# Performance work log

Measured on AMD Instinct MI355X. Metric: run time of the kernel, lower is better.

Reference implementation:

```python
import jax, jax.numpy as jnp
import numpy as np

B, H, W, D, K = 16, 64, 64, 128, 4096


def setup_inputs() -> dict:
    key = jax.random.key(0)
    k1, k2 = jax.random.split(key)
    z = jax.random.normal(k1, (B, H, W, D), dtype=jnp.float32)
    emb = jax.random.normal(k2, (K, D), dtype=jnp.float32)
    return {"z": z, "emb": emb}


def reference(z, emb):
    # z: [B,H,W,D] pre-quantized features (channels-last, as in the torch code
    # after permute(0,2,3,1)); emb: [K,D] codebook.
    d = z.shape[-1]
    zf = z.reshape(-1, d)  # [N,D]
    # squared euclidean distances: ||z||^2 + ||e||^2 - 2 z.e
    dists = (jnp.sum(zf * zf, axis=1, keepdims=True)
             + jnp.sum(emb * emb, axis=1)
             - 2.0 * zf @ emb.T)  # [N,K]
    idx = jnp.argmin(dists, axis=1)  # [N]
    # one-hot @ emb in the original == direct gather (same math)
    z_q = jnp.take(emb, idx, axis=0).reshape(z.shape)  # [B,H,W,D]
    codebook_loss = jnp.mean((jax.lax.stop_gradient(z_q) - z) ** 2)
    commitment_loss = jnp.mean((z_q - jax.lax.stop_gradient(z)) ** 2)
    loss = codebook_loss + 0.25 * commitment_loss
    # straight-through estimator
    z_q_st = z + jax.lax.stop_gradient(z_q - z)
    z_q_out = jnp.transpose(z_q_st, (0, 3, 1, 2))  # [B,D,H,W]
    return z_q_out, loss
```

## Files before the change

### kernel.cpp

```cpp
#include <hip/hip_runtime.h>

#define NB 16
#define NH 64
#define NW 64
#define ND 128
#define NK 4096
#define NROWS (NB * NH * NW)
#define OUT_ELEMS (NB * ND * NH * NW)
#define MARGIN_F 0.10f

typedef _Float16 f16x8 __attribute__((ext_vector_type(8)));
typedef float f32x4 __attribute__((ext_vector_type(4)));

__device__ __forceinline__ unsigned short f2h(float x) {
    _Float16 h = (_Float16)x;
    return __builtin_bit_cast(unsigned short, h);
}
__device__ __forceinline__ unsigned long long pack_si(float s, int idx) {
    unsigned int u = __float_as_uint(s);
    unsigned int key = ((int)u < 0) ? ~u : (u | 0x80000000u);
    return ((unsigned long long)key << 32) | (unsigned int)idx;
}

__global__ void emb_prep_kernel(const float* __restrict__ emb,
                                float* __restrict__ enorm,
                                unsigned short* __restrict__ e_h) {
    int wave = (blockIdx.x * blockDim.x + threadIdx.x) >> 6;
    int lane = threadIdx.x & 63;
    if (wave >= NK) return;
    const float* e = emb + (size_t)wave * ND;
    float a = e[lane];
    float b = e[lane + 64];
    const int m = (wave & 7) << 3;
    e_h[(size_t)wave * ND + (lane ^ m)] = f2h(a);
    e_h[(size_t)wave * ND + ((lane + 64) ^ m)] = f2h(b);
    float s = a * a + b * b;
#pragma unroll
    for (int off = 32; off > 0; off >>= 1) s += __shfl_down(s, off, 64);
    if (lane == 0) enorm[wave] = s;
}

#define ZST 136

__global__ void
__attribute__((amdgpu_flat_work_group_size(256, 256)))
mfma_argmin_kernel(const float* __restrict__ z,
                   const unsigned short* __restrict__ e_h,
                   const float* __restrict__ enorm,
                   int* __restrict__ idx_out,
                   int* __restrict__ rcount,
                   int* __restrict__ rlist,
                   unsigned long long* __restrict__ rpart) {
    __shared__ alignas(16) unsigned short ubuf[2 * 64 * ND];
    __shared__ float redb1[2 * 64];
    __shared__ float redb2[2 * 64];
    __shared__ int   redi1[2 * 64];

    const int bid = blockIdx.x;
    const int rowbase = bid * 64;
    const int t = threadIdx.x;
    const int lane = t & 63;
    const int wid = __builtin_amdgcn_readfirstlane(t >> 6);

    const float4* zg = (const float4*)(z + (size_t)rowbase * ND);
#pragma unroll
    for (int q = 0; q < 8; q++) {
        int i = t + 256 * q;
        float4 v = zg[i];
        int r = i >> 5;
        int c4 = (i & 31) << 2;
        ushort4 hv = make_ushort4(f2h(v.x), f2h(v.y), f2h(v.z), f2h(v.w));
        *(ushort4*)&ubuf[r * ZST + c4] = hv;
    }
    __syncthreads();

    const int quad = lane >> 4;
    const int c = lane & 15;
    const int rh = wid >> 1;
    const int ch = wid & 1;

    f16x8 ar[2][4];
#pragma unroll
    for (int mi = 0; mi < 2; mi++)
#pragma unroll
        for (int kk = 0; kk < 4; kk++)
            ar[mi][kk] = *(const f16x8*)&ubuf[(rh * 32 + mi * 16 + c) * ZST + quad * 8 + kk * 32];
    __syncthreads();

#pragma unroll
    for (int j = 0; j < 4; j++) {
        int seg = (wid << 2) + j;
        __builtin_amdgcn_global_load_lds(
            (const unsigned int*)(e_h + seg * 512 + lane * 8),
            (unsigned int*)&ubuf[seg * 512], 16, 0, 0);
    }
    float en0 = enorm[ch * 32 + c];
    float en1 = enorm[ch * 32 + 16 + c];
    __syncthreads();

    const int bswz = (c & 7) << 3;
    const int bbase0 = (ch * 32 + c) * ND;

    float b1[2][4], b2[2][4];
    int i1[2][4];
#pragma unroll
    for (int mi = 0; mi < 2; mi++)
#pragma unroll
        for (int r = 0; r < 4; r++) { b1[mi][r] = -3.4e38f; b2[mi][r] = -3.4e38f; i1[mi][r] = 0; }

    for (int ts = 0; ts < NK / 64; ts++) {
        const int cur = ts & 1;
        const int curoff = cur << 13;

        float nen0 = 0.f, nen1 = 0.f;
        if (ts < NK / 64 - 1) {
            nen0 = enorm[(ts + 1) * 64 + ch * 32 + c];
            nen1 = enorm[(ts + 1) * 64 + ch * 32 + 16 + c];
            const unsigned short* gt = e_h + (size_t)(ts + 1) * (64 * ND);
#pragma unroll
            for (int j = 0; j < 4; j++) {
                int seg = (wid << 2) + j;
                __builtin_amdgcn_global_load_lds(
                    (const unsigned int*)(gt + seg * 512 + lane * 8),
                    (unsigned int*)&ubuf[(curoff ^ 8192) + seg * 512], 16, 0, 0);
            }
        }

        const float h0 = -0.5f * en0;
        const float h1 = -0.5f * en1;
        f32x4 acc[2][2];
#pragma unroll
        for (int mi = 0; mi < 2; mi++) {
            acc[mi][0] = (f32x4){h0, h0, h0, h0};
            acc[mi][1] = (f32x4){h1, h1, h1, h1};
        }

#pragma unroll
        for (int kk = 0; kk < 4; kk++) {
            const int doff = (quad * 8 + kk * 32) ^ bswz;
            f16x8 bv0 = *(const f16x8*)&ubuf[curoff + bbase0 + doff];
            f16x8 bv1 = *(const f16x8*)&ubuf[curoff + bbase0 + 16 * ND + doff];
            acc[0][0] = __builtin_amdgcn_mfma_f32_16x16x32_f16(ar[0][kk], bv0, acc[0][0], 0, 0, 0);
            acc[0][1] = __builtin_amdgcn_mfma_f32_16x16x32_f16(ar[0][kk], bv1, acc[0][1], 0, 0, 0);
            acc[1][0] = __builtin_amdgcn_mfma_f32_16x16x32_f16(ar[1][kk], bv0, acc[1][0], 0, 0, 0);
            acc[1][1] = __builtin_amdgcn_mfma_f32_16x16x32_f16(ar[1][kk], bv1, acc[1][1], 0, 0, 0);
        }

#pragma unroll
        for (int ni = 0; ni < 2; ni++) {
            const int n = ts * 64 + ch * 32 + ni * 16 + c;
#pragma unroll
            for (int mi = 0; mi < 2; mi++)
#pragma unroll
                for (int r = 0; r < 4; r++) {
                    float q = acc[mi][ni][r];
                    b2[mi][r] = fmaxf(b2[mi][r], fminf(b1[mi][r], q));
                    i1[mi][r] = (q > b1[mi][r]) ? n : i1[mi][r];
                    b1[mi][r] = fmaxf(b1[mi][r], q);
                }
        }

        __syncthreads();
        en0 = nen0;
        en1 = nen1;
    }

#pragma unroll
    for (int off = 1; off < 16; off <<= 1) {
#pragma unroll
        for (int mi = 0; mi < 2; mi++)
#pragma unroll
            for (int r = 0; r < 4; r++) {
                float ob1 = __shfl_xor(b1[mi][r], off, 64);
                float ob2 = __shfl_xor(b2[mi][r], off, 64);
                int oi1 = __shfl_xor(i1[mi][r], off, 64);
                float hi = fmaxf(b1[mi][r], ob1);
                float lo = fminf(b1[mi][r], ob1);
                b2[mi][r] = fmaxf(fmaxf(b2[mi][r], ob2), lo);
                i1[mi][r] = (ob1 > b1[mi][r]) ? oi1 : i1[mi][r];
                b1[mi][r] = hi;
            }
    }

    if (c == 0) {
#pragma unroll
        for (int mi = 0; mi < 2; mi++)
#pragma unroll
            for (int r = 0; r < 4; r++) {
                int rowl = rh * 32 + mi * 16 + quad * 4 + r;
                redb1[ch * 64 + rowl] = b1[mi][r];
                redb2[ch * 64 + rowl] = b2[mi][r];
                redi1[ch * 64 + rowl] = i1[mi][r];
            }
    }
    __syncthreads();

    if (t < 64) {
        float B1 = redb1[t], B2 = redb2[t];
        int I1 = redi1[t];
        float ob1 = redb1[64 + t];
        float ob2 = redb2[64 + t];
        int oi1 = redi1[64 + t];
        float hi = fmaxf(B1, ob1);
        float lo = fminf(B1, ob1);
        B2 = fmaxf(fmaxf(B2, ob2), lo);
        I1 = (ob1 > B1) ? oi1 : I1;
        B1 = hi;
        idx_out[rowbase + t] = I1;
        if (2.0f * (B1 - B2) < MARGIN_F) {
            rpart[rowbase + t] = ~0ull;
            int p = atomicAdd(rcount, 1);
            rlist[p] = rowbase + t;
        }
    }
}

#define RR 8
#define SC 512
#define CH 64

__global__ void __launch_bounds__(256, 2)
rescue_kernel(const float* __restrict__ z,
              const float* __restrict__ emb,
              const float* __restrict__ enorm,
              const int* __restrict__ rcount,
              const int* __restrict__ rlist,
              unsigned long long* __restrict__ rpart) {
    __shared__ float2 ze[RR * 64];
    __shared__ float2 es[64 * 65];
    __shared__ int ids[RR];

    const int t = threadIdx.x;
    const int cnt = *rcount;
    if (cnt == 0) return;
    const int ngrp = (cnt + RR - 1) / RR;
    const int nwork = ngrp * 8;

    const int r = t >> 6;
    const int cl = t & 63;

    for (int g = blockIdx.x; g < nwork; g += gridDim.x) {
        const int gi = g >> 3;
        const int slice = g & 7;

        if (t < RR) {
            int j = gi * RR + t;
            ids[t] = rlist[j < cnt ? j : cnt - 1];
        }
        __syncthreads();
        const int rowA = ids[r];
        const int rowB = ids[r + 4];
#pragma unroll
        for (int q2 = 0; q2 < 2; q2++) {
            int i = t + 256 * q2;
            int rr = i >> 6;
            int d2 = i & 63;
            ze[rr * 64 + d2] = ((const float2*)(z + (size_t)ids[rr] * ND))[d2];
        }

        unsigned long long bestA = ~0ull, bestB = ~0ull;
        const int kbase = slice * SC;

        for (int ch2 = 0; ch2 < SC / CH; ch2++) {
            __syncthreads();
#pragma unroll
            for (int q = 0; q < 16; q++) {
                int i = t + 256 * q;
                int code = i >> 6;
                int d2 = i & 63;
                float2 v = ((const float2*)(emb + (size_t)(kbase + ch2 * CH + code) * ND))[d2];
                es[d2 * 65 + code] = v;
            }
            __syncthreads();

            int k = kbase + ch2 * CH + cl;
            float a0 = 0.f, a1 = 0.f, a2 = 0.f, a3 = 0.f;
            float c0 = 0.f, c1 = 0.f, c2 = 0.f, c3 = 0.f;
#pragma unroll
            for (int d2 = 0; d2 < 64; d2 += 2) {
                float2 ev0 = es[d2 * 65 + cl];
                float2 ev1 = es[(d2 + 1) * 65 + cl];
                float2 zA0 = ze[r * 64 + d2];
                float2 zA1 = ze[r * 64 + d2 + 1];
                float2 zB0 = ze[(r + 4) * 64 + d2];
                float2 zB1 = ze[(r + 4) * 64 + d2 + 1];
                a0 = fmaf(zA0.x, ev0.x, a0);
                a1 = fmaf(zA0.y, ev0.y, a1);
                a2 = fmaf(zA1.x, ev1.x, a2);
                a3 = fmaf(zA1.y, ev1.y, a3);
                c0 = fmaf(zB0.x, ev0.x, c0);
                c1 = fmaf(zB0.y, ev0.y, c1);
                c2 = fmaf(zB1.x, ev1.x, c2);
                c3 = fmaf(zB1.y, ev1.y, c3);
            }
            float sA = fmaf(-2.0f, (a0 + a1) + (a2 + a3), enorm[k]);
            float sB = fmaf(-2.0f, (c0 + c1) + (c2 + c3), enorm[k]);
            unsigned long long pA = pack_si(sA, k);
            unsigned long long pB = pack_si(sB, k);
            bestA = (pA < bestA) ? pA : bestA;
            bestB = (pB < bestB) ? pB : bestB;
        }

#pragma unroll
        for (int off = 32; off > 0; off >>= 1) {
            unsigned long long oA = __shfl_down(bestA, off, 64);
            unsigned long long oB = __shfl_down(bestB, off, 64);
            bestA = (oA < bestA) ? oA : bestA;
            bestB = (oB < bestB) ? oB : bestB;
        }
        if (cl == 0) {
            atomicMin(&rpart[rowA], bestA);
            atomicMin(&rpart[rowB], bestB);
        }
        __syncthreads();
    }
}

__global__ void rescue_fin_kernel(const int* __restrict__ rcount,
                                  const int* __restrict__ rlist,
                                  const unsigned long long* __restrict__ rpart,
                                  int* __restrict__ idx_out) {
    const int cnt = *rcount;
    for (int i = blockIdx.x * blockDim.x + threadIdx.x; i < cnt;
         i += gridDim.x * blockDim.x) {
        int row = rlist[i];
        idx_out[row] = (int)(rpart[row] & 0xffffffffull);
    }
}

__global__ void out_kernel(const float* __restrict__ z,
                           const float* __restrict__ emb,
                           const int* __restrict__ idx,
                           float* __restrict__ out,
                           float* __restrict__ losspart) {
    __shared__ float zq[64 * 129];
    __shared__ int ids[64];
    __shared__ float redl[4];

    const int bid = blockIdx.x;
    const int b = bid >> 6;
    const int h = bid & 63;
    const int rowbase = bid * 64;
    const int t = threadIdx.x;

    if (t < 64) ids[t] = idx[rowbase + t];
    __syncthreads();

    const int d = t & 127;
    const int w0 = t >> 7;
    float lsum = 0.f;
#pragma unroll
    for (int wq = 0; wq < 32; wq++) {
        int w = w0 + 2 * wq;
        float e = emb[(size_t)ids[w] * ND + d];
        float zv = z[((size_t)(rowbase + w)) * ND + d];
        float df = e - zv;
        lsum = fmaf(df, df, lsum);
        zq[w * 129 + d] = e;
    }
#pragma unroll
    for (int off = 32; off > 0; off >>= 1) lsum += __shfl_down(lsum, off, 64);
    if ((t & 63) == 0) redl[t >> 6] = lsum;
    __syncthreads();
    if (t == 0) losspart[bid] = redl[0] + redl[1] + redl[2] + redl[3];

    const int w = t & 63;
    const int dq = t >> 6;
#pragma unroll
    for (int dd0 = 0; dd0 < 32; dd0++) {
        int dd = dq + 4 * dd0;
        out[(((size_t)b * ND + dd) * NH + h) * NW + w] = zq[w * 129 + dd];
    }
}

__global__ void loss_kernel(const float* __restrict__ losspart,
                            float* __restrict__ out) {
    __shared__ float redl[4];
    const int t = threadIdx.x;
    float s = 0.f;
#pragma unroll
    for (int i = 0; i < 4; i++) s += losspart[t + 256 * i];
#pragma unroll
    for (int off = 32; off > 0; off >>= 1) s += __shfl_down(s, off, 64);
    if ((t & 63) == 0) redl[t >> 6] = s;
    __syncthreads();
    if (t == 0) {
        float total = redl[0] + redl[1] + redl[2] + redl[3];
        out[OUT_ELEMS] = 1.25f * total / (float)OUT_ELEMS;
    }
}

extern "C" void kernel_launch(void* const* d_in, const int* in_sizes, int n_in,
                              void* d_out, int out_size, void* d_ws, size_t ws_size,
                              hipStream_t stream) {
    const float* z = (const float*)d_in[0];
    const float* emb = (const float*)d_in[1];
    float* out = (float*)d_out;

    char* ws = (char*)d_ws;
    int* ws_idx = (int*)ws;
    float* ws_enorm = (float*)(ws + (256 << 10));
    float* ws_losspart = (float*)(ws + (272 << 10));
    int* ws_rcount = (int*)(ws + (276 << 10));
    int* ws_rlist = (int*)(ws + (277 << 10));
    unsigned short* ws_eh = (unsigned short*)(ws + (533 << 10));
    unsigned long long* ws_rpart = (unsigned long long*)(ws + (1557 << 10));

    hipMemsetAsync(ws_rcount, 0, sizeof(int), stream);
    emb_prep_kernel<<<NK / 4, 256, 0, stream>>>(emb, ws_enorm, ws_eh);
    mfma_argmin_kernel<<<NROWS / 64, 256, 0, stream>>>(z, ws_eh, ws_enorm,
                                                       ws_idx, ws_rcount,
                                                       ws_rlist, ws_rpart);
    rescue_kernel<<<2048, 256, 0, stream>>>(z, emb, ws_enorm, ws_rcount,
                                            ws_rlist, ws_rpart);
    rescue_fin_kernel<<<64, 256, 0, stream>>>(ws_rcount, ws_rlist, ws_rpart,
                                              ws_idx);
    out_kernel<<<NB * NH, 256, 0, stream>>>(z, emb, ws_idx, out, ws_losspart);
    loss_kernel<<<1, 256, 0, stream>>>(ws_losspart, out);
}
```

Measured before the change: 325.9 us.

## Pre-transpose codebook and double-buffer rescue tiles via direct global-to-LDS loads

Adds a kernel that transposes the fp32 codebook into a d-major float2 layout once. The rescue kernel then streams 64-code chunks from it straight into LDS with global_load_lds, double-buffered so the next chunk loads while the current one is computed. This replaces the per-chunk register-staged transposed store and removes one barrier per chunk. In exchange it costs an extra launch, about 2 MB of transpose traffic, and doubled LDS use. It also drops the launch-bounds occupancy hint.

```diff
diff --git a/kernel.cpp b/kernel.cpp
--- a/kernel.cpp
+++ b/kernel.cpp
@@ -38,6 +38,28 @@
 #pragma unroll
     for (int off = 32; off > 0; off >>= 1) s += __shfl_down(s, off, 64);
     if (lane == 0) enorm[wave] = s;
+}
+
+__global__ void transp_kernel(const float* __restrict__ emb,
+                              float2* __restrict__ emb_t) {
+    __shared__ float2 tile[64 * 65];
+    const int cb = blockIdx.x * 64;
+    const int t = threadIdx.x;
+#pragma unroll
+    for (int q = 0; q < 16; q++) {
+        int i = t + 256 * q;
+        int code = i >> 6;
+        int d2 = i & 63;
+        tile[code * 65 + d2] = ((const float2*)(emb + (size_t)(cb + code) * ND))[d2];
+    }
+    __syncthreads();
+#pragma unroll
+    for (int q = 0; q < 16; q++) {
+        int i = t + 256 * q;
+        int d2 = i >> 6;
+        int code = i & 63;
+        emb_t[(size_t)d2 * NK + cb + code] = tile[code * 65 + d2];
+    }
 }
 
 #define ZST 136
@@ -219,15 +241,15 @@
 #define SC 512
 #define CH 64
 
-__global__ void __launch_bounds__(256, 2)
+__global__ void
 rescue_kernel(const float* __restrict__ z,
-              const float* __restrict__ emb,
+              const float2* __restrict__ emb_t,
               const float* __restrict__ enorm,
               const int* __restrict__ rcount,
               const int* __restrict__ rlist,
               unsigned long long* __restrict__ rpart) {
+    __shared__ alignas(16) float2 es[2][64 * 64];
     __shared__ float2 ze[RR * 64];
-    __shared__ float2 es[64 * 65];
     __shared__ int ids[RR];
 
     const int t = threadIdx.x;
@@ -258,28 +280,40 @@
             ze[rr * 64 + d2] = ((const float2*)(z + (size_t)ids[rr] * ND))[d2];
         }
 
+        const int kbase = slice * SC;
+#pragma unroll
+        for (int j = 0; j < 8; j++) {
+            int seg = r * 8 + j;
+            const float2* src = emb_t + (size_t)(seg * 2 + (cl >> 5)) * NK
+                                + kbase + (cl & 31) * 2;
+            __builtin_amdgcn_global_load_lds((const unsigned int*)src,
+                (unsigned int*)&es[0][seg * 128], 16, 0, 0);
+        }
+        __syncthreads();
+
         unsigned long long bestA = ~0ull, bestB = ~0ull;
-        const int kbase = slice * SC;
 
         for (int ch2 = 0; ch2 < SC / CH; ch2++) {
-            __syncthreads();
-#pragma unroll
-            for (int q = 0; q < 16; q++) {
-                int i = t + 256 * q;
-                int code = i >> 6;
-                int d2 = i & 63;
-                float2 v = ((const float2*)(emb + (size_t)(kbase + ch2 * CH + code) * ND))[d2];
-                es[d2 * 65 + code] = v;
+            const int bi = ch2 & 1;
+            if (ch2 < SC / CH - 1) {
+                const int kb2 = kbase + (ch2 + 1) * CH;
+#pragma unroll
+                for (int j = 0; j < 8; j++) {
+                    int seg = r * 8 + j;
+                    const float2* src = emb_t + (size_t)(seg * 2 + (cl >> 5)) * NK
+                                        + kb2 + (cl & 31) * 2;
+                    __builtin_amdgcn_global_load_lds((const unsigned int*)src,
+                        (unsigned int*)&es[bi ^ 1][seg * 128], 16, 0, 0);
+                }
             }
-            __syncthreads();
 
             int k = kbase + ch2 * CH + cl;
             float a0 = 0.f, a1 = 0.f, a2 = 0.f, a3 = 0.f;
             float c0 = 0.f, c1 = 0.f, c2 = 0.f, c3 = 0.f;
 #pragma unroll
             for (int d2 = 0; d2 < 64; d2 += 2) {
-                float2 ev0 = es[d2 * 65 + cl];
-                float2 ev1 = es[(d2 + 1) * 65 + cl];
+                float2 ev0 = es[bi][d2 * 64 + cl];
+                float2 ev1 = es[bi][(d2 + 1) * 64 + cl];
                 float2 zA0 = ze[r * 64 + d2];
                 float2 zA1 = ze[r * 64 + d2 + 1];
                 float2 zB0 = ze[(r + 4) * 64 + d2];
@@ -299,6 +333,8 @@
             unsigned long long pB = pack_si(sB, k);
             bestA = (pA < bestA) ? pA : bestA;
             bestB = (pB < bestB) ? pB : bestB;
+
+            __syncthreads();
         }
 
 #pragma unroll
@@ -312,7 +348,6 @@
             atomicMin(&rpart[rowA], bestA);
             atomicMin(&rpart[rowB], bestB);
         }
-        __syncthreads();
     }
 }
 
@@ -405,13 +440,15 @@
     int* ws_rlist = (int*)(ws + (277 << 10));
     unsigned short* ws_eh = (unsigned short*)(ws + (533 << 10));
     unsigned long long* ws_rpart = (unsigned long long*)(ws + (1557 << 10));
+    float2* ws_embt = (float2*)(ws + (2069 << 10));
 
     hipMemsetAsync(ws_rcount, 0, sizeof(int), stream);
     emb_prep_kernel<<<NK / 4, 256, 0, stream>>>(emb, ws_enorm, ws_eh);
+    transp_kernel<<<NK / 64, 256, 0, stream>>>(emb, ws_embt);
     mfma_argmin_kernel<<<NROWS / 64, 256, 0, stream>>>(z, ws_eh, ws_enorm,
                                                        ws_idx, ws_rcount,
                                                        ws_rlist, ws_rpart);
-    rescue_kernel<<<2048, 256, 0, stream>>>(z, emb, ws_enorm, ws_rcount,
+    rescue_kernel<<<2048, 256, 0, stream>>>(z, ws_embt, ws_enorm, ws_rcount,
                                             ws_rlist, ws_rpart);
     rescue_fin_kernel<<<64, 256, 0, stream>>>(ws_rcount, ws_rlist, ws_rpart,
                                               ws_idx);
```

Measured after the change: 482.9 us. +48.2%, slower.
